# Optimization experiments

Hardware: AMD Instinct MI355X
Metric: run time of the kernel (lower is better)

Reference implementation:

```python
import math
import jax, jax.numpy as jnp
import numpy as np

N_HEADS = 8

def setup_inputs() -> dict:
    key = jax.random.key(0)
    qkv = jax.random.normal(key, (4, 3 * N_HEADS * 64, 2048), dtype=jnp.float32)
    return {"qkv": qkv}

def reference(qkv) -> jnp.ndarray:
    bs, width, length = qkv.shape
    assert width % (3 * N_HEADS) == 0
    ch = width // (3 * N_HEADS)
    q, k, v = jnp.split(qkv, 3, axis=1)            # each [N, H*C, T]
    scale = 1.0 / math.sqrt(math.sqrt(ch))
    qh = (q * scale).reshape(bs * N_HEADS, ch, length)  # [BH, C, T]
    kh = (k * scale).reshape(bs * N_HEADS, ch, length)
    vh = v.reshape(bs * N_HEADS, ch, length)
    weight = jnp.einsum('bct,bcs->bts', qh, kh)    # [BH, T, T]
    weight = jax.nn.softmax(weight.astype(jnp.float32), axis=-1).astype(weight.dtype)
    a = jnp.einsum('bts,bcs->bct', weight, vh)     # [BH, C, T]
    return a.reshape(bs, -1, length)
```

## Files before the change

kernel.cpp:

```cpp
#include <hip/hip_runtime.h>

#define T_LEN 2048
#define CH 64
#define NH 8
#define STILE 64
#define TTILE 256
#define WT 32
#define NIT (T_LEN / STILE)
#define CSK 68
#define CS 72
#define QS 260
#define RS 68

#define QSCALE 0.180336880972948929f

typedef __attribute__((ext_vector_type(4))) float  f32x4;
typedef __attribute__((ext_vector_type(8))) __bf16 bf16x8;
typedef __attribute__((ext_vector_type(4))) __bf16 bf16x4;
typedef __attribute__((ext_vector_type(2))) __bf16 bf16x2;
typedef __attribute__((ext_vector_type(2))) unsigned int uint2v;
typedef __attribute__((ext_vector_type(4))) unsigned int uint4v;

union SMem {
  float qstage[CH * QS];
  struct {
    __bf16 k_hi[2][STILE * CSK];
    __bf16 v_s [2][CH * CS];
  } loop;
  struct {
    float o[8][WT][RS];
    float l[2][8][4][16];
  } red;
};

#define MFMA(A, B, C) __builtin_amdgcn_mfma_f32_16x16x32_bf16((A), (B), (C), 0, 0, 0)

__device__ __forceinline__ unsigned pkbf2(float lo, float hi) {
  bf16x2 t = {(__bf16)lo, (__bf16)hi};
  return __builtin_bit_cast(unsigned, t);
}

__device__ __forceinline__ void load_k(const float* kp, int s0, int ltid, float2 (&kreg)[4]) {
  int cq  = ltid >> 5;
  int sp2 = ltid & 31;
  const float* kc = kp + (size_t)(4 * cq) * T_LEN + s0 + 2 * sp2;
#pragma unroll
  for (int r = 0; r < 4; ++r)
    kreg[r] = *(const float2*)(kc + (size_t)r * T_LEN);
}

__device__ __forceinline__ void store_k(__bf16* kh, int ltid, const float2 (&kreg)[4]) {
  int cq  = ltid >> 5;
  int sp2 = ltid & 31;
  bf16x4 w0 = {(__bf16)kreg[0].x, (__bf16)kreg[1].x, (__bf16)kreg[2].x, (__bf16)kreg[3].x};
  bf16x4 w1 = {(__bf16)kreg[0].y, (__bf16)kreg[1].y, (__bf16)kreg[2].y, (__bf16)kreg[3].y};
  *(bf16x4*)&kh[(2 * sp2 + 0) * CSK + 4 * cq] = w0;
  *(bf16x4*)&kh[(2 * sp2 + 1) * CSK + 4 * cq] = w1;
}

__device__ __forceinline__ void load_v(const float* vp, int s0, int ltid, f32x4 (&vreg)[2]) {
#pragma unroll
  for (int rr = 0; rr < 2; ++rr) {
    int fidx = rr * 512 + ltid;
    int c  = fidx >> 4;
    int s4 = (fidx & 15) << 2;
    vreg[rr] = *(const f32x4*)(vp + (size_t)c * T_LEN + s0 + s4);
  }
}

__device__ __forceinline__ void store_v(__bf16* vs, int ltid, const f32x4 (&vreg)[2]) {
#pragma unroll
  for (int rr = 0; rr < 2; ++rr) {
    int fidx = rr * 512 + ltid;
    int c  = fidx >> 4;
    int s4 = (fidx & 15) << 2;
    bf16x4 vv = {(__bf16)vreg[rr].x, (__bf16)vreg[rr].y,
                 (__bf16)vreg[rr].z, (__bf16)vreg[rr].w};
    *(bf16x4*)&vs[c * CS + s4] = vv;
  }
}

__global__ __launch_bounds__(1024, 4)
void qkv_attn_mfma(const float* __restrict__ qkv, float* __restrict__ out) {
  __shared__ SMem sm;
  const int tid  = threadIdx.x;
  const int lane = tid & 63;
  const int wave = tid >> 6;
  const int wt   = wave & 7;
  const int ws   = wave >> 3;
  const int tn   = lane & 15;
  const int quad = lane >> 4;
  const int stid = tid & 511;

  const int d0 = blockIdx.x;
  const int w  = ((d0 & 7) << 5) | (d0 >> 3);
  const int ttile = w & 7;
  const int bh    = w >> 3;
  const int b = bh >> 3, h = bh & 7;
  const size_t base = (size_t)b * (3 * NH * CH) * T_LEN;
  const float* qp = qkv + base + (size_t)(CH * h) * T_LEN;
  const float* kp = qkv + base + (size_t)(CH * (NH + h)) * T_LEN;
  const float* vp = qkv + base + (size_t)(CH * (2 * NH + h)) * T_LEN;
  const int t0 = ttile * TTILE;

#pragma unroll
  for (int rr = 0; rr < 4; ++rr) {
    int fidx = rr * 1024 + tid;
    int c  = fidx >> 6;
    int t4 = (fidx & 63) << 2;
    f32x4 q4 = *(const f32x4*)(qp + (size_t)c * T_LEN + t0 + t4);
    *(f32x4*)&sm.qstage[c * QS + t4] = q4;
  }
  __syncthreads();

  bf16x8 qh[2][2];
#pragma unroll
  for (int nb = 0; nb < 2; ++nb)
#pragma unroll
    for (int kb = 0; kb < 2; ++kb) {
      int tloc = wt * WT + nb * 16 + tn;
      bf16x8 H;
#pragma unroll
      for (int j = 0; j < 8; ++j) {
        float qv = sm.qstage[(kb * 32 + quad * 8 + j) * QS + tloc] * QSCALE;
        H[j] = (__bf16)qv;
      }
      qh[nb][kb] = H;
    }
  __syncthreads();

  f32x4 acc[4][2];
  float l_part[2] = {0.f, 0.f};
#pragma unroll
  for (int mbc = 0; mbc < 4; ++mbc)
#pragma unroll
    for (int nb = 0; nb < 2; ++nb)
      acc[mbc][nb] = (f32x4){0.f, 0.f, 0.f, 0.f};

  float2 kreg[4];
  f32x4  vreg[2];
  if (ws == 0) { load_k(kp, 0, stid, kreg); store_k(sm.loop.k_hi[0], stid, kreg); }
  else         { load_v(vp, 0, stid, vreg); store_v(sm.loop.v_s[0], stid, vreg); }
  __syncthreads();

  for (int it = 0; it < NIT; ++it) {
    const int cur = it & 1;
    const bool more = (it + 1 < NIT);

    if (more) {
      if (ws == 0) load_k(kp, (it + 1) * STILE, stid, kreg);
      else         load_v(vp, (it + 1) * STILE, stid, vreg);
    }

    const __bf16* kh = sm.loop.k_hi[cur];
    bf16x8 ah[2][2];
#pragma unroll
    for (int mb = 0; mb < 2; ++mb) {
      const int srow = (32 * ws + 16 * mb + tn) * CSK;
#pragma unroll
      for (int kb = 0; kb < 2; ++kb) {
        bf16x4 a0 = *(const bf16x4*)&kh[srow + 32 * kb + quad * 8];
        bf16x4 a1 = *(const bf16x4*)&kh[srow + 32 * kb + quad * 8 + 4];
        ah[mb][kb] = __builtin_shufflevector(a0, a1, 0, 1, 2, 3, 4, 5, 6, 7);
      }
    }
    f32x4 d[2][2];
#pragma unroll
    for (int mb = 0; mb < 2; ++mb)
#pragma unroll
      for (int nb = 0; nb < 2; ++nb) {
        f32x4 t = (f32x4){0.f, 0.f, 0.f, 0.f};
        t = MFMA(ah[mb][0], qh[nb][0], t);
        t = MFMA(ah[mb][1], qh[nb][1], t);
        d[mb][nb] = t;
      }

    const __bf16* vs = sm.loop.v_s[cur];
    bf16x8 av[4];
#pragma unroll
    for (int mbc = 0; mbc < 4; ++mbc)
      av[mbc] = *(const bf16x8*)&vs[(16 * mbc + tn) * CS + 32 * ws + quad * 8];

    bf16x8 bp[2];
#pragma unroll
    for (int nb = 0; nb < 2; ++nb) {
      float rs = 0.f;
#pragma unroll
      for (int mb = 0; mb < 2; ++mb)
#pragma unroll
        for (int r = 0; r < 4; ++r) {
          float e = __builtin_amdgcn_exp2f(d[mb][nb][r]);
          d[mb][nb][r] = e;
          rs += e;
        }
      l_part[nb] += rs;
      unsigned u00 = pkbf2(d[0][nb][0], d[0][nb][1]);
      unsigned u01 = pkbf2(d[0][nb][2], d[0][nb][3]);
      unsigned u10 = pkbf2(d[1][nb][0], d[1][nb][1]);
      unsigned u11 = pkbf2(d[1][nb][2], d[1][nb][3]);
      uint2v s0 = __builtin_amdgcn_permlane32_swap(u00, u10, false, false);
      uint2v r0 = __builtin_amdgcn_permlane16_swap(s0.x, s0.y, false, false);
      uint2v s1 = __builtin_amdgcn_permlane32_swap(u01, u11, false, false);
      uint2v r1 = __builtin_amdgcn_permlane16_swap(s1.x, s1.y, false, false);
      uint4v wv = {r0.x, r1.x, r0.y, r1.y};
      bp[nb] = __builtin_bit_cast(bf16x8, wv);
    }

#pragma unroll
    for (int mbc = 0; mbc < 4; ++mbc)
#pragma unroll
      for (int nb = 0; nb < 2; ++nb)
        acc[mbc][nb] = MFMA(av[mbc], bp[nb], acc[mbc][nb]);

    if (more) {
      if (ws == 0) store_k(sm.loop.k_hi[cur ^ 1], stid, kreg);
      else         store_v(sm.loop.v_s [cur ^ 1], stid, vreg);
    }
    __syncthreads();
  }

  if (ws == 1) {
#pragma unroll
    for (int nb = 0; nb < 2; ++nb) {
      sm.red.l[nb][wt][quad][tn] = l_part[nb];
#pragma unroll
      for (int mbc = 0; mbc < 4; ++mbc)
        *(f32x4*)&sm.red.o[wt][nb * 16 + tn][16 * mbc + quad * 4] = acc[mbc][nb];
    }
  }
  __syncthreads();
  if (ws == 0) {
    float* op = out + (size_t)bh * CH * T_LEN;
#pragma unroll
    for (int nb = 0; nb < 2; ++nb) {
      float l = l_part[nb] + sm.red.l[nb][wt][quad][tn];
      l += __shfl_xor(l, 16, 64);
      l += __shfl_xor(l, 32, 64);
      float inv_l = 1.0f / l;
      int t = t0 + wt * WT + nb * 16 + tn;
#pragma unroll
      for (int mbc = 0; mbc < 4; ++mbc) {
        f32x4 o = acc[mbc][nb] + *(const f32x4*)&sm.red.o[wt][nb * 16 + tn][16 * mbc + quad * 4];
        o = o * inv_l;
        int c = 16 * mbc + quad * 4;
        op[(size_t)(c + 0) * T_LEN + t] = o.x;
        op[(size_t)(c + 1) * T_LEN + t] = o.y;
        op[(size_t)(c + 2) * T_LEN + t] = o.z;
        op[(size_t)(c + 3) * T_LEN + t] = o.w;
      }
    }
  }
}

extern "C" void kernel_launch(void* const* d_in, const int* in_sizes, int n_in,
                              void* d_out, int out_size, void* d_ws, size_t ws_size,
                              hipStream_t stream) {
  const float* qkv = (const float*)d_in[0];
  float* out = (float*)d_out;
  dim3 grid(256);
  qkv_attn_mfma<<<grid, 1024, 0, stream>>>(qkv, out);
}
```

Baseline: 120.0 us.

## Software-pipeline PV MFMA one tile behind with triple-buffered V tiles

Defers the P·V MFMA for each tile to the next iteration so it can overlap the current tile's QK MFMAs, exp and permlane packing. V shared buffers go from double to triple buffering so the previous tile stays resident, with a drain step after the loop. This adds register pressure from the carried P fragments, but it fits in the existing union footprint.

```diff
diff --git a/kernel.cpp b/kernel.cpp
--- a/kernel.cpp
+++ b/kernel.cpp
@@ -25,7 +25,7 @@
   float qstage[CH * QS];
   struct {
     __bf16 k_hi[2][STILE * CSK];
-    __bf16 v_s [2][CH * CS];
+    __bf16 v_s [3][CH * CS];
   } loop;
   struct {
     float o[8][WT][RS];
@@ -143,6 +143,10 @@
   else         { load_v(vp, 0, stid, vreg); store_v(sm.loop.v_s[0], stid, vreg); }
   __syncthreads();
 
+  bf16x8 bp_prev[2];
+  int vprev = 2;
+  int vst   = 1;
+
   for (int it = 0; it < NIT; ++it) {
     const int cur = it & 1;
     const bool more = (it + 1 < NIT);
@@ -175,13 +179,19 @@
         d[mb][nb] = t;
       }
 
-    const __bf16* vs = sm.loop.v_s[cur];
-    bf16x8 av[4];
-#pragma unroll
-    for (int mbc = 0; mbc < 4; ++mbc)
-      av[mbc] = *(const bf16x8*)&vs[(16 * mbc + tn) * CS + 32 * ws + quad * 8];
-
-    bf16x8 bp[2];
+    if (it > 0) {
+      const __bf16* vsp = sm.loop.v_s[vprev];
+      bf16x8 av[4];
+#pragma unroll
+      for (int mbc = 0; mbc < 4; ++mbc)
+        av[mbc] = *(const bf16x8*)&vsp[(16 * mbc + tn) * CS + 32 * ws + quad * 8];
+#pragma unroll
+      for (int mbc = 0; mbc < 4; ++mbc)
+#pragma unroll
+        for (int nb = 0; nb < 2; ++nb)
+          acc[mbc][nb] = MFMA(av[mbc], bp_prev[nb], acc[mbc][nb]);
+    }
+
 #pragma unroll
     for (int nb = 0; nb < 2; ++nb) {
       float rs = 0.f;
@@ -203,21 +213,31 @@
       uint2v s1 = __builtin_amdgcn_permlane32_swap(u01, u11, false, false);
       uint2v r1 = __builtin_amdgcn_permlane16_swap(s1.x, s1.y, false, false);
       uint4v wv = {r0.x, r1.x, r0.y, r1.y};
-      bp[nb] = __builtin_bit_cast(bf16x8, wv);
-    }
-
-#pragma unroll
-    for (int mbc = 0; mbc < 4; ++mbc)
-#pragma unroll
-      for (int nb = 0; nb < 2; ++nb)
-        acc[mbc][nb] = MFMA(av[mbc], bp[nb], acc[mbc][nb]);
+      bp_prev[nb] = __builtin_bit_cast(bf16x8, wv);
+    }
 
     if (more) {
       if (ws == 0) store_k(sm.loop.k_hi[cur ^ 1], stid, kreg);
-      else         store_v(sm.loop.v_s [cur ^ 1], stid, vreg);
-    }
+      else         store_v(sm.loop.v_s [vst],     stid, vreg);
+    }
+    vprev = (vprev == 2) ? 0 : vprev + 1;
+    vst   = (vst   == 2) ? 0 : vst   + 1;
     __syncthreads();
   }
+
+  {
+    const __bf16* vsp = sm.loop.v_s[vprev];
+    bf16x8 av[4];
+#pragma unroll
+    for (int mbc = 0; mbc < 4; ++mbc)
+      av[mbc] = *(const bf16x8*)&vsp[(16 * mbc + tn) * CS + 32 * ws + quad * 8];
+#pragma unroll
+    for (int mbc = 0; mbc < 4; ++mbc)
+#pragma unroll
+      for (int nb = 0; nb < 2; ++nb)
+        acc[mbc][nb] = MFMA(av[mbc], bp_prev[nb], acc[mbc][nb]);
+  }
+  __syncthreads();
 
   if (ws == 1) {
 #pragma unroll
```

Result: no change. 118.3 us (-1.4%).
